# Kernel optimization log

Hardware: AMD Instinct MI355X
Metric: run time of the kernel (lower is better)

## Reference

```python
import jax, jax.numpy as jnp
import numpy as np

B, L = 2048, 8192
IN, H, OUT = 128, 512, 10
N_FRAMES = L // IN  # frame_step == frame_size -> non-overlapping unfold == reshape


def _lstm_layer(xs, W_ih, W_hh, b):
    """xs: [T, B, D_in]; returns (hs [T, B, H], h_T [B, H]).
    PyTorch gate order: i, f, g, o."""
    Bsz = xs.shape[1]
    h0 = jnp.zeros((Bsz, H), xs.dtype)
    c0 = jnp.zeros((Bsz, H), xs.dtype)

    def step(carry, x_t):
        h, c = carry
        gates = x_t @ W_ih.T + h @ W_hh.T + b  # [B, 4H]
        i, f, g, o = jnp.split(gates, 4, axis=-1)
        c = jax.nn.sigmoid(f) * c + jax.nn.sigmoid(i) * jnp.tanh(g)
        h = jax.nn.sigmoid(o) * jnp.tanh(c)
        return (h, c), h

    (hT, _), hs = jax.lax.scan(step, (h0, c0), xs)
    return hs, hT


def setup_inputs() -> dict:
    key = jax.random.key(0)
    ks = jax.random.split(key, 12)
    s_in = 1.0 / np.sqrt(H)
    return {
        "xb": jax.random.normal(ks[0], (B, L), jnp.float32),
        "W_ih0": jax.random.normal(ks[1], (4 * H, IN), jnp.float32) * s_in,
        "W_hh0": jax.random.normal(ks[2], (4 * H, H), jnp.float32) * s_in,
        "b0": jax.random.normal(ks[3], (4 * H,), jnp.float32) * s_in,
        "W_ih1": jax.random.normal(ks[4], (4 * H, H), jnp.float32) * s_in,
        "W_hh1": jax.random.normal(ks[5], (4 * H, H), jnp.float32) * s_in,
        "b1": jax.random.normal(ks[6], (4 * H,), jnp.float32) * s_in,
        "W_out": jax.random.normal(ks[7], (OUT, H), jnp.float32) * s_in,
        "b_out": jax.random.normal(ks[8], (OUT,), jnp.float32) * s_in,
    }


def reference(xb, W_ih0, W_hh0, b0, W_ih1, W_hh1, b1, W_out, b_out):
    # unfold(1, fs, fs) with step==size -> reshape; transpose to time-major
    frames = xb.reshape(B, N_FRAMES, IN).transpose(1, 0, 2)  # [T, B, IN]
    hs0, _ = _lstm_layer(frames, W_ih0, W_hh0, b0)           # [T, B, H]
    _, hT1 = _lstm_layer(hs0, W_ih1, W_hh1, b1)              # [B, H]
    return hT1 @ W_out.T + b_out                             # [B, OUT]
```

## Files before the change

### kernel.cpp

```cpp
#include <hip/hip_runtime.h>
#include <hip/hip_bf16.h>


typedef _Float16 f16x8 __attribute__((ext_vector_type(8)));
typedef float f32x4 __attribute__((ext_vector_type(4)));

#define Bsz 2048
#define Lsz 8192
#define Tsz 64

__global__ void cvt_f32_f16(const float* __restrict__ src, _Float16* __restrict__ dst, int n4) {
    int stride = gridDim.x * blockDim.x;
    for (int i = blockIdx.x * blockDim.x + threadIdx.x; i < n4; i += stride) {
        float4 v = ((const float4*)src)[i];
        union { _Float16 h[4]; ushort4 u; } o;
        o.h[0] = (_Float16)v.x; o.h[1] = (_Float16)v.y;
        o.h[2] = (_Float16)v.z; o.h[3] = (_Float16)v.w;
        ((ushort4*)dst)[i] = o.u;
    }
}

__global__ void pack_w(const float* __restrict__ Wih, const float* __restrict__ Whh,
                       _Float16* __restrict__ dst, int K1) {
    int KT = K1 + 512;
    int n4 = 2048 * KT / 4;
    int stride = gridDim.x * blockDim.x;
    for (int i = blockIdx.x * blockDim.x + threadIdx.x; i < n4; i += stride) {
        int row = i / (KT / 4);
        int col = (i % (KT / 4)) * 4;
        const float* s = (col < K1) ? (Wih + (size_t)row * K1 + col)
                                    : (Whh + (size_t)row * 512 + (col - K1));
        float4 v = *(const float4*)s;
        union { _Float16 h[4]; ushort4 u; } o;
        o.h[0] = (_Float16)v.x; o.h[1] = (_Float16)v.y;
        o.h[2] = (_Float16)v.z; o.h[3] = (_Float16)v.w;
        ((ushort4*)dst)[i] = o.u;
    }
}

__device__ __forceinline__ float fsig(float x)  { return 1.0f / (1.0f + __expf(-x)); }
__device__ __forceinline__ float ftanh(float x) { return 1.0f - 2.0f / (__expf(2.0f * x) + 1.0f); }

__device__ __forceinline__ void gll16(const _Float16* src, char* dst) {
    __builtin_amdgcn_global_load_lds(
        (const __attribute__((address_space(1))) void*)src,
        (__attribute__((address_space(3))) void*)dst, 16, 0, 0);
}

template<int K1>
__device__ __forceinline__ void stageB(
    const _Float16* __restrict__ Wcat, int cb, int k0, char* buf, int tid)
{
    constexpr int KT = K1 + 512;
#pragma unroll
    for (int qq = 0; qq < 4; ++qq) {
        const int j  = qq * 32 + (tid >> 3);
        const int cg = (((tid & 7) ^ (j & 7)) << 3);
        const int wrow = ((j >> 4) & 3) * 512 + cb * 32 + (j >> 6) * 16 + (j & 15);
        gll16(Wcat + (size_t)wrow * KT + k0 + cg, buf + qq * 4096 + (tid >> 6) * 1024);
    }
}

template<int K1>
__device__ __forceinline__ void stageA(
    const _Float16* __restrict__ A1, int lda1,
    const _Float16* __restrict__ A2,
    int rowtile, int k0, char* buf, int tid)
{
#pragma unroll
    for (int qq = 0; qq < 4; ++qq) {
        const int row  = qq * 32 + (tid >> 3);
        const int cg   = (((tid & 7) ^ (row & 7)) << 3);
        const int brow = rowtile * 128 + row;
        char* d = buf + qq * 4096 + (tid >> 6) * 1024;
        if (k0 < K1) gll16(A1 + (size_t)brow * lda1 + k0 + cg, d);
        else         gll16(A2 + (size_t)brow * 512 + (k0 - K1) + cg, d);
    }
}

template<int K1>
__device__ __forceinline__ void step_v17(
    const _Float16* __restrict__ A1, int lda1,
    const _Float16* __restrict__ A2,
    const _Float16* __restrict__ Wcat,
    const float* __restrict__ bias,
    float* __restrict__ c,
    _Float16* __restrict__ h_out,
    int rowtile, int cb, char* lds)
{
    constexpr int KT  = K1 + 512;
    constexpr int NIT = KT / 64;
    const int tid = threadIdx.x;
    const int ln  = tid & 63;
    const int wv  = tid >> 6;
    const int llo = ln & 15, lhi = ln >> 4;
    const int wr  = wv >> 1, wc = wv & 1;

    f32x4 acc[4][4] = {};

    stageA<K1>(A1, lda1, A2, rowtile, 0, lds + 32768, tid);
    stageB<K1>(Wcat, cb, 0, lds, tid);

    for (int it = 0; it < NIT; ++it) {
        if (it + 1 < NIT) {
            stageB<K1>(Wcat, cb, (it + 1) * 64, lds + ((it + 1) & 1) * 16384, tid);
            stageA<K1>(A1, lda1, A2, rowtile, (it + 1) * 64,
                       lds + 32768 + ((it + 1) & 1) * 16384, tid);
        }
        if (it < NIT - 1) asm volatile("s_waitcnt vmcnt(8)" ::: "memory");
        else              asm volatile("s_waitcnt vmcnt(0)" ::: "memory");
        __builtin_amdgcn_s_barrier();
        __builtin_amdgcn_sched_barrier(0);

        char* bb = lds + (it & 1) * 16384;
        char* ab = lds + 32768 + (it & 1) * 16384;
#pragma unroll
        for (int ks = 0; ks < 2; ++ks) {
            const int gsw = (((ks * 4 + lhi) ^ (llo & 7)) << 4);
            f16x8 a[4], b[4];
#pragma unroll
            for (int mi = 0; mi < 4; ++mi)
                a[mi] = *(const f16x8*)(ab + (wr * 64 + mi * 16 + llo) * 128 + gsw);
#pragma unroll
            for (int cf = 0; cf < 4; ++cf)
                b[cf] = *(const f16x8*)(bb + (wc * 64 + cf * 16 + llo) * 128 + gsw);
#pragma unroll
            for (int mi = 0; mi < 4; ++mi)
#pragma unroll
                for (int cf = 0; cf < 4; ++cf)
                    acc[mi][cf] = __builtin_amdgcn_mfma_f32_16x16x32_f16(
                        a[mi], b[cf], acc[mi][cf], 0, 0, 0);
        }
        __builtin_amdgcn_s_barrier();
        __builtin_amdgcn_sched_barrier(0);
    }

    const int hcol = cb * 32 + wc * 16 + llo;
    float bz[4];
#pragma unroll
    for (int g = 0; g < 4; ++g) bz[g] = bias[g * 512 + hcol];
#pragma unroll
    for (int mi = 0; mi < 4; ++mi)
#pragma unroll
        for (int rr = 0; rr < 4; ++rr) {
            const int row = rowtile * 128 + wr * 64 + mi * 16 + lhi * 4 + rr;
            const size_t idx = (size_t)row * 512 + hcol;
            float iv = acc[mi][0][rr] + bz[0];
            float fv = acc[mi][1][rr] + bz[1];
            float gv = acc[mi][2][rr] + bz[2];
            float ov = acc[mi][3][rr] + bz[3];
            float cn = fsig(fv) * c[idx] + fsig(iv) * ftanh(gv);
            c[idx] = cn;
            float hn = fsig(ov) * ftanh(cn);
            h_out[idx] = (_Float16)hn;
        }
}

__global__ __launch_bounds__(256) void lstm_round(
    int t0, int t1,
    const _Float16* __restrict__ xb16,
    const _Float16* __restrict__ Wc0, const float* __restrict__ b0, float* __restrict__ c0,
    _Float16* __restrict__ h00, _Float16* __restrict__ h01,
    const _Float16* __restrict__ Wc1, const float* __restrict__ b1, float* __restrict__ c1,
    _Float16* __restrict__ h10, _Float16* __restrict__ h11)
{
    __shared__ __align__(16) char lds[65536];
    const int bid     = blockIdx.x;
    const int layer   = bid >> 8;
    const int lb      = bid & 255;
    const int x       = lb & 7;
    const int rest    = lb >> 3;
    const int cb      = x * 2 + (rest & 1);
    const int rowtile = rest >> 1;

    if (layer == 0) {
        if (t0 < 0) return;
        const _Float16* hr = (t0 & 1) ? h01 : h00;
        _Float16*       hw = (t0 & 1) ? h00 : h01;
        step_v17<128>(xb16 + (size_t)t0 * 128, Lsz, hr, Wc0, b0, c0, hw, rowtile, cb, lds);
    } else {
        if (t1 < 0) return;
        const _Float16* h0in = ((t1 + 1) & 1) ? h01 : h00;
        const _Float16* hr   = (t1 & 1) ? h11 : h10;
        _Float16*       hw   = (t1 & 1) ? h10 : h11;
        step_v17<512>(h0in, 512, hr, Wc1, b1, c1, hw, rowtile, cb, lds);
    }
}

__global__ void proj_kernel(const _Float16* __restrict__ h1,
                            const float* __restrict__ Wout,
                            const float* __restrict__ bout,
                            float* __restrict__ out)
{
    int tid = blockIdx.x * blockDim.x + threadIdx.x;
    if (tid >= Bsz * 10) return;
    int b = tid / 10, o = tid % 10;
    float s = bout[o];
    const _Float16* hrow = h1 + (size_t)b * 512;
    const float* wrow = Wout + (size_t)o * 512;
    for (int k = 0; k < 512; ++k) s += (float)hrow[k] * wrow[k];
    out[tid] = s;
}

extern "C" void kernel_launch(void* const* d_in, const int* in_sizes, int n_in,
                              void* d_out, int out_size, void* d_ws, size_t ws_size,
                              hipStream_t stream) {
    const float* xb    = (const float*)d_in[0];
    const float* W_ih0 = (const float*)d_in[1];
    const float* W_hh0 = (const float*)d_in[2];
    const float* b0    = (const float*)d_in[3];
    const float* W_ih1 = (const float*)d_in[4];
    const float* W_hh1 = (const float*)d_in[5];
    const float* b1    = (const float*)d_in[6];
    const float* W_out = (const float*)d_in[7];
    const float* b_out = (const float*)d_in[8];
    float* out = (float*)d_out;

    char* ws = (char*)d_ws;
    size_t off = 0;
    auto alloc = [&](size_t bytes) -> void* {
        void* p = ws + off;
        off += (bytes + 255) & ~(size_t)255;
        return p;
    };
    _Float16* xb16 = (_Float16*)alloc((size_t)Bsz * Lsz * 2);
    _Float16* Wc0  = (_Float16*)alloc((size_t)2048 * 640 * 2);
    _Float16* Wc1  = (_Float16*)alloc((size_t)2048 * 1024 * 2);
    _Float16* h00  = (_Float16*)alloc((size_t)Bsz * 512 * 2);
    _Float16* h01  = (_Float16*)alloc((size_t)Bsz * 512 * 2);
    _Float16* h10  = (_Float16*)alloc((size_t)Bsz * 512 * 2);
    _Float16* h11  = (_Float16*)alloc((size_t)Bsz * 512 * 2);
    float* c0 = (float*)alloc((size_t)Bsz * 512 * 4);
    float* c1 = (float*)alloc((size_t)Bsz * 512 * 4);

    cvt_f32_f16<<<2048, 256, 0, stream>>>(xb, xb16, Bsz * Lsz / 4);
    pack_w<<<1280, 256, 0, stream>>>(W_ih0, W_hh0, Wc0, 128);
    pack_w<<<2048, 256, 0, stream>>>(W_ih1, W_hh1, Wc1, 512);

    hipMemsetAsync(h00, 0, (size_t)Bsz * 512 * 2, stream);
    hipMemsetAsync(h10, 0, (size_t)Bsz * 512 * 2, stream);
    hipMemsetAsync(c0, 0, (size_t)Bsz * 512 * 4, stream);
    hipMemsetAsync(c1, 0, (size_t)Bsz * 512 * 4, stream);

    for (int r = 0; r <= Tsz; ++r) {
        int t0 = (r < Tsz) ? r : -1;
        int t1 = r - 1;
        lstm_round<<<dim3(512), 256, 0, stream>>>(t0, t1,
            xb16, Wc0, b0, c0, h00, h01,
            Wc1, b1, c1, h10, h11);
    }

    proj_kernel<<<(Bsz * 10 + 255) / 256, 256, 0, stream>>>(h10, W_out, b_out, out);
}
```

Baseline: 1.442 ms.

## Load A operand directly to registers, halving LDS and double-buffering in VGPRs

The activation (A) tile is no longer staged through LDS. Each lane loads its MFMA A fragments straight from global memory into registers, double-buffered across two unrolled iteration bodies, while the weight (B) tile stays in LDS. This removes the LDS writes and reads for A and halves shared memory to 32KB, which could allow more blocks per CU. In exchange it adds register pressure from the second fragment set and uses less-coalesced 16-byte per-lane global reads, with the load latency now exposed against the MFMA work.

```diff
diff --git a/kernel.cpp b/kernel.cpp
--- a/kernel.cpp
+++ b/kernel.cpp
@@ -62,24 +62,61 @@
 }
 
 template<int K1>
-__device__ __forceinline__ void stageA(
-    const _Float16* __restrict__ A1, int lda1,
-    const _Float16* __restrict__ A2,
-    int rowtile, int k0, char* buf, int tid)
-{
-#pragma unroll
-    for (int qq = 0; qq < 4; ++qq) {
-        const int row  = qq * 32 + (tid >> 3);
-        const int cg   = (((tid & 7) ^ (row & 7)) << 3);
-        const int brow = rowtile * 128 + row;
-        char* d = buf + qq * 4096 + (tid >> 6) * 1024;
-        if (k0 < K1) gll16(A1 + (size_t)brow * lda1 + k0 + cg, d);
-        else         gll16(A2 + (size_t)brow * 512 + (k0 - K1) + cg, d);
-    }
-}
-
-template<int K1>
-__device__ __forceinline__ void step_v17(
+__device__ __forceinline__ void loadA(
+    f16x8 (*aX)[2],
+    const _Float16* const* a1row, const _Float16* const* a2row,
+    int it, int lhi)
+{
+#pragma unroll
+    for (int ks = 0; ks < 2; ++ks) {
+        const int k = it * 64 + ks * 32 + lhi * 8;
+#pragma unroll
+        for (int mi = 0; mi < 4; ++mi)
+            aX[mi][ks] = (k < K1) ? *(const f16x8*)(a1row[mi] + k)
+                                  : *(const f16x8*)(a2row[mi] + (k - K1));
+    }
+}
+
+template<int K1>
+__device__ __forceinline__ void iter_body(
+    int it, f16x8 (*aU)[2], f16x8 (*aL)[2],
+    const _Float16* const* a1row, const _Float16* const* a2row,
+    const _Float16* __restrict__ Wcat, int cb, char* lds, int tid,
+    int lhi, int llo, int wc, f32x4 (*acc)[4])
+{
+    constexpr int KT  = K1 + 512;
+    constexpr int NIT = KT / 64;
+    if (it + 1 < NIT)
+        stageB<K1>(Wcat, cb, (it + 1) * 64, lds + ((it + 1) & 1) * 16384, tid);
+    if (it < NIT - 1) asm volatile("s_waitcnt vmcnt(4)" ::: "memory");
+    else              asm volatile("s_waitcnt vmcnt(0)" ::: "memory");
+    __builtin_amdgcn_s_barrier();
+    __builtin_amdgcn_sched_barrier(0);
+
+    if (it + 1 < NIT)
+        loadA<K1>(aL, a1row, a2row, it + 1, lhi);
+
+    char* bb = lds + (it & 1) * 16384;
+#pragma unroll
+    for (int ks = 0; ks < 2; ++ks) {
+        const int gsw = (((ks * 4 + lhi) ^ (llo & 7)) << 4);
+        f16x8 b[4];
+#pragma unroll
+        for (int cf = 0; cf < 4; ++cf)
+            b[cf] = *(const f16x8*)(bb + (wc * 64 + cf * 16 + llo) * 128 + gsw);
+#pragma unroll
+        for (int mi = 0; mi < 4; ++mi)
+#pragma unroll
+            for (int cf = 0; cf < 4; ++cf)
+                acc[mi][cf] = __builtin_amdgcn_mfma_f32_16x16x32_f16(
+                    aU[mi][ks], b[cf], acc[mi][cf], 0, 0, 0);
+    }
+    __builtin_amdgcn_s_barrier();
+    __builtin_amdgcn_sched_barrier(0);
+}
+
+template<int K1>
+__device__ __forceinline__ void step_v18(
     const _Float16* __restrict__ A1, int lda1,
     const _Float16* __restrict__ A2,
     const _Float16* __restrict__ Wcat,
@@ -90,6 +127,7 @@
 {
     constexpr int KT  = K1 + 512;
     constexpr int NIT = KT / 64;
+    static_assert(NIT % 2 == 0, "even NIT for 2-body unroll");
     const int tid = threadIdx.x;
     const int ln  = tid & 63;
     const int wv  = tid >> 6;
@@ -98,41 +136,23 @@
 
     f32x4 acc[4][4] = {};
 
-    stageA<K1>(A1, lda1, A2, rowtile, 0, lds + 32768, tid);
+    const _Float16* a1row[4];
+    const _Float16* a2row[4];
+#pragma unroll
+    for (int mi = 0; mi < 4; ++mi) {
+        const int row = rowtile * 128 + wr * 64 + mi * 16 + llo;
+        a1row[mi] = A1 + (size_t)row * lda1;
+        a2row[mi] = A2 + (size_t)row * 512;
+    }
+
+    f16x8 aP[4][2], aQ[4][2];
+
+    loadA<K1>(aP, a1row, a2row, 0, lhi);
     stageB<K1>(Wcat, cb, 0, lds, tid);
 
-    for (int it = 0; it < NIT; ++it) {
-        if (it + 1 < NIT) {
-            stageB<K1>(Wcat, cb, (it + 1) * 64, lds + ((it + 1) & 1) * 16384, tid);
-            stageA<K1>(A1, lda1, A2, rowtile, (it + 1) * 64,
-                       lds + 32768 + ((it + 1) & 1) * 16384, tid);
-        }
-        if (it < NIT - 1) asm volatile("s_waitcnt vmcnt(8)" ::: "memory");
-        else              asm volatile("s_waitcnt vmcnt(0)" ::: "memory");
-        __builtin_amdgcn_s_barrier();
-        __builtin_amdgcn_sched_barrier(0);
-
-        char* bb = lds + (it & 1) * 16384;
-        char* ab = lds + 32768 + (it & 1) * 16384;
-#pragma unroll
-        for (int ks = 0; ks < 2; ++ks) {
-            const int gsw = (((ks * 4 + lhi) ^ (llo & 7)) << 4);
-            f16x8 a[4], b[4];
-#pragma unroll
-            for (int mi = 0; mi < 4; ++mi)
-                a[mi] = *(const f16x8*)(ab + (wr * 64 + mi * 16 + llo) * 128 + gsw);
-#pragma unroll
-            for (int cf = 0; cf < 4; ++cf)
-                b[cf] = *(const f16x8*)(bb + (wc * 64 + cf * 16 + llo) * 128 + gsw);
-#pragma unroll
-            for (int mi = 0; mi < 4; ++mi)
-#pragma unroll
-                for (int cf = 0; cf < 4; ++cf)
-                    acc[mi][cf] = __builtin_amdgcn_mfma_f32_16x16x32_f16(
-                        a[mi], b[cf], acc[mi][cf], 0, 0, 0);
-        }
-        __builtin_amdgcn_s_barrier();
-        __builtin_amdgcn_sched_barrier(0);
+    for (int it2 = 0; it2 < NIT; it2 += 2) {
+        iter_body<K1>(it2,     aP, aQ, a1row, a2row, Wcat, cb, lds, tid, lhi, llo, wc, acc);
+        iter_body<K1>(it2 + 1, aQ, aP, a1row, a2row, Wcat, cb, lds, tid, lhi, llo, wc, acc);
     }
 
     const int hcol = cb * 32 + wc * 16 + llo;
@@ -164,7 +184,7 @@
     const _Float16* __restrict__ Wc1, const float* __restrict__ b1, float* __restrict__ c1,
     _Float16* __restrict__ h10, _Float16* __restrict__ h11)
 {
-    __shared__ __align__(16) char lds[65536];
+    __shared__ __align__(16) char lds[32768];
     const int bid     = blockIdx.x;
     const int layer   = bid >> 8;
     const int lb      = bid & 255;
@@ -177,13 +197,13 @@
         if (t0 < 0) return;
         const _Float16* hr = (t0 & 1) ? h01 : h00;
         _Float16*       hw = (t0 & 1) ? h00 : h01;
-        step_v17<128>(xb16 + (size_t)t0 * 128, Lsz, hr, Wc0, b0, c0, hw, rowtile, cb, lds);
+        step_v18<128>(xb16 + (size_t)t0 * 128, Lsz, hr, Wc0, b0, c0, hw, rowtile, cb, lds);
     } else {
         if (t1 < 0) return;
         const _Float16* h0in = ((t1 + 1) & 1) ? h01 : h00;
         const _Float16* hr   = (t1 & 1) ? h11 : h10;
         _Float16*       hw   = (t1 & 1) ? h10 : h11;
-        step_v17<512>(h0in, 512, hr, Wc1, b1, c1, hw, rowtile, cb, lds);
+        step_v18<512>(h0in, 512, hr, Wc1, b1, c1, hw, rowtile, cb, lds);
     }
 }
 
```

Result: slower. 2.329 ms (+61.5%).
